# Kernel tuning notes

Hardware: AMD Instinct MI355X
Metric: run time of the kernel (lower is better)

The kernel has to match this reference:

```python
import jax, jax.numpy as jnp
import numpy as np

B, T, C = 16, 512, 1024
D, K, W = 4096, 128, 8


def _scatter_topk(a, k, use_values):
    """Top-k along last axis; return dense array with top-k values (or 1.0) scattered, zeros elsewhere."""
    shp = a.shape
    a2 = a.reshape(-1, shp[-1])
    vals, idx = jax.lax.top_k(a2, k)
    rows = jnp.arange(a2.shape[0])[:, None]
    src = vals if use_values else jnp.ones_like(vals)
    return jnp.zeros_like(a2).at[rows, idx].set(src).reshape(shp)


def _window_topk(x, k, window_size):
    # x: (B, T, D)
    b, t, d = x.shape
    stride = max(1, window_size // 2)
    if stride >= t:
        num_windows, pad, t_pad = 1, 0, t
    else:
        num_windows = (t - window_size) // stride + 1
        required = (num_windows - 1) * stride + window_size
        pad = max(0, required - t)
        t_pad = t + pad
    if pad > 0:
        x = jnp.pad(x, ((0, 0), (0, pad), (0, 0)))
    starts = jnp.arange(num_windows) * stride                      # (NW,)
    tidx = starts[:, None] + jnp.arange(window_size)               # (NW, W)
    x_windows = x[:, tidx, :]                                      # (B, NW, W, D)
    window_sums = x_windows.sum(axis=2)                            # (B, NW, D)
    mask_windows = _scatter_topk(window_sums, k, use_values=False)  # (B, NW, D)
    votes = (x_windows * mask_windows[:, :, None, :]).reshape(b, num_windows * window_size, d)
    feature_votes = jnp.zeros((b, t_pad, d), x.dtype).at[:, tidx.reshape(-1)].add(votes)
    mask_combined = _scatter_topk(feature_votes, k, use_values=False)  # (B, Tp, D)
    x_sparse = x * mask_combined
    return x_sparse[:, :t - 0, :] if pad > 0 else x_sparse


def setup_inputs() -> dict:
    key = jax.random.key(0)
    ks = jax.random.split(key, 4)
    x_ssl = jax.random.normal(ks[0], (B, T, C), jnp.float32)
    W_dec = jax.random.normal(ks[1], (C, D), jnp.float32)
    W_dec = W_dec / jnp.linalg.norm(W_dec, axis=0, keepdims=True)
    W_enc = W_dec.T                                                # tied init, as in module
    W1 = jax.random.normal(ks[2], (256, D), jnp.float32) * (1.0 / np.sqrt(D))
    W2 = jax.random.normal(ks[3], (2, 256), jnp.float32) * (1.0 / np.sqrt(256))
    return dict(
        x_ssl=x_ssl, W_enc=W_enc, b_enc=jnp.zeros((D,), jnp.float32),
        W_dec=W_dec, b_dec=jnp.zeros((C,), jnp.float32),
        ln_g=jnp.ones((D,), jnp.float32), ln_b=jnp.zeros((D,), jnp.float32),
        W1=W1, b1=jnp.zeros((256,), jnp.float32),
        W2=W2, b2=jnp.zeros((2,), jnp.float32),
    )


def reference(x_ssl, W_enc, b_enc, W_dec, b_dec, ln_g, ln_b, W1, b1, W2, b2):
    b, t, c = x_ssl.shape
    x_flat = x_ssl.reshape(b * t, c)
    # SAE encode with window top-k (window_size=8 > 1 path)
    pre = jnp.einsum('nc,dc->nd', x_flat - b_dec, W_enc) + b_enc
    post_relu = jax.nn.relu(pre).reshape(b, t, -1)                 # (B, T, D)
    encoded = _window_topk(post_relu, K, W)                        # (B, T, D)
    encoded_flat = encoded.reshape(b * t, -1)
    # SAE decode + reconstruction loss
    x_recon = jnp.einsum('nd,cd->nc', encoded_flat, W_dec) + b_dec
    sae_loss = jnp.mean((x_recon - x_flat) ** 2)
    # classifier on pooled sparse features (dropout is inference no-op)
    pooled = encoded.mean(axis=1)                                  # (B, D) == AdaptiveAvgPool1d(1)
    mu = pooled.mean(axis=-1, keepdims=True)
    var = pooled.var(axis=-1, keepdims=True)
    ln = (pooled - mu) / jnp.sqrt(var + 1e-5) * ln_g + ln_b
    h = jax.nn.relu(ln @ W1.T + b1)
    logits = h @ W2.T + b2
    log_probs = jax.nn.log_softmax(logits, axis=-1)
    return log_probs, sae_loss
```

## Files before the change

### kernel.cpp

```cpp
#include <hip/hip_runtime.h>

#define BB   16
#define TT   512
#define CC   1024
#define DD   4096
#define NN   (BB*TT)
#define NWIN 127
#define KTOP 128

typedef __attribute__((ext_vector_type(8))) unsigned short ushort8;
typedef _Float16 half8 __attribute__((ext_vector_type(8)));
typedef __attribute__((ext_vector_type(4))) float f32x4;

__device__ __forceinline__ unsigned short f2h(float f) {
    union { _Float16 h; unsigned short u; } c;
    c.h = (_Float16)f;
    return c.u;
}
__device__ __forceinline__ float h2f(unsigned short u) {
    union { unsigned short u; _Float16 h; } c;
    c.u = u;
    return (float)c.h;
}
__device__ __forceinline__ unsigned tokey(float f) {
    unsigned u = __float_as_uint(f);
    return (u & 0x80000000u) ? ~u : (u | 0x80000000u);
}
__device__ __forceinline__ void async_lds16(const void* g, void* l) {
    __builtin_amdgcn_global_load_lds((const __attribute__((address_space(1))) void*)g,
                                     (__attribute__((address_space(3))) void*)l, 16, 0, 0);
}

#define PH_SYNC() do { __builtin_amdgcn_sched_barrier(0); __builtin_amdgcn_s_barrier(); \
                       asm volatile("s_waitcnt lgkmcnt(0)" ::: "memory"); \
                       __builtin_amdgcn_sched_barrier(0); __builtin_amdgcn_s_setprio(1); } while (0)
#define PH_END()  do { __builtin_amdgcn_s_setprio(0); __builtin_amdgcn_sched_barrier(0); \
                       __builtin_amdgcn_s_barrier(); } while (0)

__device__ __forceinline__ unsigned wave_prefix_incl(unsigned v) {
    int lane = threadIdx.x & 63;
#pragma unroll
    for (int off = 1; off < 64; off <<= 1) {
        unsigned n = __shfl_up(v, off, 64);
        if (lane >= off) v += n;
    }
    return v;
}
__device__ __forceinline__ unsigned wave_suffix_incl(unsigned v) {
    int lane = threadIdx.x & 63;
#pragma unroll
    for (int off = 1; off < 64; off <<= 1) {
        unsigned n = __shfl_down(v, off, 64);
        if (lane + off < 64) v += n;
    }
    return v;
}

__device__ __forceinline__ unsigned select_top128(const unsigned* keys,
                                                  unsigned* hist, unsigned* shx) {
    const int tid = threadIdx.x, wid = tid >> 6, lane = tid & 63;
    const unsigned ZKEY = 0x80000000u;
    unsigned cpos = 0, cz = 0;
#pragma unroll
    for (int i = 0; i < 16; ++i) {
        cpos += (keys[i] > ZKEY);
        cz   += (keys[i] == ZKEY);
    }
    unsigned ppos = wave_prefix_incl(cpos);
    unsigned pz   = wave_prefix_incl(cz);
    if (lane == 63) { shx[wid] = ppos; shx[4 + wid] = pz; }
    __syncthreads();
    unsigned nz = shx[0] + shx[1] + shx[2] + shx[3];
    unsigned selbits = 0u;
    if (nz <= KTOP) {
        unsigned need = KTOP - nz;
        unsigned zr = pz - cz;
        if (wid > 0) zr += shx[4];
        if (wid > 1) zr += shx[5];
        if (wid > 2) zr += shx[6];
#pragma unroll
        for (int i = 0; i < 16; ++i) {
            bool sel = (keys[i] > ZKEY) || (keys[i] == ZKEY && zr < need);
            if (keys[i] == ZKEY) ++zr;
            selbits |= (sel ? 1u : 0u) << i;
        }
        return selbits;
    }
    unsigned k2[16];
#pragma unroll
    for (int i = 0; i < 16; ++i) k2[i] = (keys[i] > ZKEY) ? keys[i] : 0u;
    unsigned prefix = 0u, pmask = 0u, Kr = KTOP;
    for (int shift = 24; shift >= 0; shift -= 8) {
        hist[tid] = 0u; hist[256 + tid] = 0u; hist[512 + tid] = 0u; hist[768 + tid] = 0u;
        __syncthreads();
        unsigned* h = hist + (wid << 8);
#pragma unroll
        for (int i = 0; i < 16; ++i)
            if (k2[i] && (k2[i] & pmask) == prefix) atomicAdd(&h[(k2[i] >> shift) & 255u], 1u);
        __syncthreads();
        unsigned v = hist[tid] + hist[256 + tid] + hist[512 + tid] + hist[768 + tid];
        unsigned s = wave_suffix_incl(v);
        if (lane == 0) shx[wid] = s;
        __syncthreads();
        unsigned stot = s;
        if (wid == 0) stot += shx[1] + shx[2] + shx[3];
        else if (wid == 1) stot += shx[2] + shx[3];
        else if (wid == 2) stot += shx[3];
        unsigned above = stot - v;
        if (stot >= Kr && above < Kr) { shx[8] = (unsigned)tid; shx[9] = Kr - above; }
        __syncthreads();
        prefix |= shx[8] << shift;
        pmask |= 0xFFu << shift;
        Kr = shx[9];
    }
    unsigned T = prefix, need = Kr;
    unsigned ce = 0;
#pragma unroll
    for (int i = 0; i < 16; ++i) ce += (k2[i] == T);
    unsigned pe = wave_prefix_incl(ce);
    __syncthreads();
    if (lane == 63) shx[4 + wid] = pe;
    __syncthreads();
    unsigned er = pe - ce;
    if (wid > 0) er += shx[4];
    if (wid > 1) er += shx[5];
    if (wid > 2) er += shx[6];
#pragma unroll
    for (int i = 0; i < 16; ++i) {
        bool sel = (k2[i] > T) || (k2[i] == T && er < need);
        if (k2[i] == T) ++er;
        selbits |= (sel ? 1u : 0u) << i;
    }
    return selbits;
}

__global__ __launch_bounds__(256) void k_convert_all(const float* __restrict__ x,
                                                     const float* __restrict__ Wenc,
                                                     const float* __restrict__ Wdec,
                                                     const float* __restrict__ bdec,
                                                     unsigned short* __restrict__ xh,
                                                     unsigned short* __restrict__ wh,
                                                     unsigned short* __restrict__ wdh,
                                                     float* __restrict__ pooled_zero) {
    const int bid = blockIdx.x;
    if (bid < 8192) {
        size_t i = (size_t)bid * 256 + threadIdx.x;
        float4 v = ((const float4*)x)[i];
        size_t c = (i * 4) & (CC - 1);
        v.x -= bdec[c]; v.y -= bdec[c + 1]; v.z -= bdec[c + 2]; v.w -= bdec[c + 3];
        uint2 o;
        o.x = (unsigned)f2h(v.x) | ((unsigned)f2h(v.y) << 16);
        o.y = (unsigned)f2h(v.z) | ((unsigned)f2h(v.w) << 16);
        ((uint2*)xh)[i] = o;
    } else if (bid < 12288) {
        size_t i = (size_t)(bid - 8192) * 256 + threadIdx.x;
        float4 v = ((const float4*)Wenc)[i];
        uint2 o;
        o.x = (unsigned)f2h(v.x) | ((unsigned)f2h(v.y) << 16);
        o.y = (unsigned)f2h(v.z) | ((unsigned)f2h(v.w) << 16);
        ((uint2*)wh)[i] = o;
    } else if (bid < 16384) {
        size_t i = (size_t)(bid - 12288) * 256 + threadIdx.x;
        float4 v = ((const float4*)Wdec)[i];
        uint2 o;
        o.x = (unsigned)f2h(v.x) | ((unsigned)f2h(v.y) << 16);
        o.y = (unsigned)f2h(v.z) | ((unsigned)f2h(v.w) << 16);
        ((uint2*)wdh)[i] = o;
    } else {
        const int n4 = (BB * DD + 64) / 4;
        for (int i = threadIdx.x; i < n4; i += 256)
            ((float4*)pooled_zero)[i] = make_float4(0.f, 0.f, 0.f, 0.f);
    }
}

__global__ __launch_bounds__(512, 2) void k_gemm_enc_256(const unsigned short* __restrict__ Ah,
                                                         const unsigned short* __restrict__ Bh,
                                                         const float* __restrict__ bias,
                                                         unsigned short* __restrict__ Cout,
                                                         float* __restrict__ gsum) {
    __shared__ __align__(16) unsigned short lds[2][4][128 * 64];
    const int tid = threadIdx.x, w = tid >> 6, lane = tid & 63;
    const int bm = blockIdx.y * 256, bn = blockIdx.x * 256;
    const int wr = w >> 2, wc = w & 3;
    const int rA = lane & 15, q = lane >> 4;
    const int sc0 = (q ^ (rA & 7)) << 3, sc1 = ((4 + q) ^ (rA & 7)) << 3;
    const int s_rt = w * 16 + (lane >> 3);
    const int s_ct = ((lane & 7) ^ (lane >> 3)) * 8;
    const unsigned short* Abase = Ah + ((size_t)(bm + s_rt)) * 1024 + s_ct;
    const unsigned short* Bbase = Bh + ((size_t)(bn + s_rt)) * 1024 + s_ct;

    auto STAGE = [&](const unsigned short* gb, int rowoff, int kt, unsigned short* reg) {
        const unsigned short* g = gb + (size_t)rowoff * 1024 + (kt << 6);
        async_lds16(g, reg + w * 1024);
        async_lds16(g + 8 * 1024, reg + w * 1024 + 512);
    };

    half8 a[4][2], b[4][2];
    f32x4 acc[8][4] = {};

    auto RDA4 = [&](const unsigned short* reg) {
#pragma unroll
        for (int mf = 0; mf < 4; ++mf) {
            const unsigned short* p = reg + (wr * 64 + mf * 16 + rA) * 64;
            a[mf][0] = *(const half8*)(p + sc0);
            a[mf][1] = *(const half8*)(p + sc1);
        }
    };
    auto RDB2 = [&](const unsigned short* reg, int nb) {
#pragma unroll
        for (int nf = 0; nf < 2; ++nf) {
            const unsigned short* p = reg + (wc * 32 + nf * 16 + rA) * 64;
            b[nb + nf][0] = *(const half8*)(p + sc0);
            b[nb + nf][1] = *(const half8*)(p + sc1);
        }
    };
    auto MF = [&](int mb, int nb) {
#pragma unroll
        for (int kk = 0; kk < 2; ++kk)
#pragma unroll
            for (int mf = 0; mf < 4; ++mf)
#pragma unroll
                for (int nf = 0; nf < 2; ++nf)
                    acc[mb + mf][nb + nf] = __builtin_amdgcn_mfma_f32_16x16x32_f16(
                        a[mf][kk], b[nb + nf][kk], acc[mb + mf][nb + nf], 0, 0, 0);
    };

    STAGE(Abase,   0, 0, lds[0][0]);
    STAGE(Bbase,   0, 0, lds[0][2]);
    STAGE(Abase, 128, 0, lds[0][1]);
    STAGE(Bbase, 128, 0, lds[0][3]);
    STAGE(Abase,   0, 1, lds[1][0]);
    STAGE(Bbase,   0, 1, lds[1][2]);
    STAGE(Abase, 128, 1, lds[1][1]);
    asm volatile("s_waitcnt vmcnt(6)" ::: "memory");
    __builtin_amdgcn_s_barrier();

    for (int i = 0; i < 8; ++i) {
        const int ko  = (2 * i + 1) & 15;
        const int ke  = (2 * i + 2) & 15;
        const int ko2 = (2 * i + 3) & 15;
        RDA4(lds[0][0]); RDB2(lds[0][2], 0);
        STAGE(Bbase, 128, ko, lds[1][3]);
        PH_SYNC(); MF(0, 0); PH_END();
        RDB2(lds[0][3], 2);
        STAGE(Abase, 0, ke, lds[0][0]);
        PH_SYNC(); MF(0, 2); PH_END();
        RDA4(lds[0][1]);
        STAGE(Bbase, 0, ke, lds[0][2]);
        PH_SYNC(); MF(4, 0); PH_END();
        STAGE(Abase, 128, ke, lds[0][1]);
        asm volatile("s_waitcnt vmcnt(6)" ::: "memory");
        PH_SYNC(); MF(4, 2); PH_END();
        RDA4(lds[1][0]); RDB2(lds[1][2], 0);
        STAGE(Bbase, 128, ke, lds[0][3]);
        PH_SYNC(); MF(0, 0); PH_END();
        RDB2(lds[1][3], 2);
        STAGE(Abase, 0, ko2, lds[1][0]);
        PH_SYNC(); MF(0, 2); PH_END();
        RDA4(lds[1][1]);
        STAGE(Bbase, 0, ko2, lds[1][2]);
        PH_SYNC(); MF(4, 0); PH_END();
        STAGE(Abase, 128, ko2, lds[1][1]);
        asm volatile("s_waitcnt vmcnt(6)" ::: "memory");
        PH_SYNC(); MF(4, 2); PH_END();
    }

    asm volatile("s_waitcnt vmcnt(0)" ::: "memory");
    __syncthreads();
    float* cbuf = (float*)&lds[0][0][0];
    const int cl = rA, qr = q * 4;
    float bv[4];
#pragma unroll
    for (int nf = 0; nf < 4; ++nf)
        bv[nf] = bias[bn + ((nf < 2) ? wc * 32 + nf * 16 : 128 + wc * 32 + (nf - 2) * 16) + cl];
    const int rg = tid >> 4, seg = tid & 15;
#pragma unroll
    for (int p = 0; p < 2; ++p) {
        if (p) __syncthreads();
#pragma unroll
        for (int mf = 0; mf < 4; ++mf) {
            int lrow0 = wr * 64 + mf * 16 + qr;
#pragma unroll
            for (int nf = 0; nf < 4; ++nf) {
                int col = ((nf < 2) ? wc * 32 + nf * 16 : 128 + wc * 32 + (nf - 2) * 16) + cl;
#pragma unroll
                for (int r = 0; r < 4; ++r) {
                    int lrow = lrow0 + r;
                    float v = acc[p * 4 + mf][nf][r] + bv[nf];
                    v = v > 0.f ? v : 0.f;
                    cbuf[lrow * 256 + (col ^ (((lrow >> 2) & 7) << 2))] = v;
                }
            }
        }
        __syncthreads();
        f32x4 gs0 = {}, gs1 = {}, gs2 = {}, gs3 = {};
#pragma unroll
        for (int i2 = 0; i2 < 4; ++i2) {
            const int lrow = rg * 4 + i2;
            const f32x4* crow = (const f32x4*)cbuf + lrow * 64;
            f32x4 v0 = crow[(seg * 4 + 0) ^ (rg & 7)];
            f32x4 v1 = crow[(seg * 4 + 1) ^ (rg & 7)];
            f32x4 v2 = crow[(seg * 4 + 2) ^ (rg & 7)];
            f32x4 v3 = crow[(seg * 4 + 3) ^ (rg & 7)];
            uint4 o0, o1;
            o0.x = (unsigned)f2h(v0[0]) | ((unsigned)f2h(v0[1]) << 16);
            o0.y = (unsigned)f2h(v0[2]) | ((unsigned)f2h(v0[3]) << 16);
            o0.z = (unsigned)f2h(v1[0]) | ((unsigned)f2h(v1[1]) << 16);
            o0.w = (unsigned)f2h(v1[2]) | ((unsigned)f2h(v1[3]) << 16);
            o1.x = (unsigned)f2h(v2[0]) | ((unsigned)f2h(v2[1]) << 16);
            o1.y = (unsigned)f2h(v2[2]) | ((unsigned)f2h(v2[3]) << 16);
            o1.z = (unsigned)f2h(v3[0]) | ((unsigned)f2h(v3[1]) << 16);
            o1.w = (unsigned)f2h(v3[2]) | ((unsigned)f2h(v3[3]) << 16);
            size_t gr = (size_t)(bm + p * 128 + lrow) * 4096 + bn + seg * 16;
            *(uint4*)&Cout[gr] = o0;
            *(uint4*)&Cout[gr + 8] = o1;
            gs0 += v0; gs1 += v1; gs2 += v2; gs3 += v3;
        }
        if (gsum) {
            size_t gr = ((size_t)(bm >> 2) + p * 32 + rg) * 4096 + bn + seg * 16;
            *(f32x4*)&gsum[gr + 0]  = gs0;
            *(f32x4*)&gsum[gr + 4]  = gs1;
            *(f32x4*)&gsum[gr + 8]  = gs2;
            *(f32x4*)&gsum[gr + 12] = gs3;
        }
    }
}

__global__ __launch_bounds__(512, 2) void k_gemm_recon_256(const unsigned short* __restrict__ Ap,
                                                           const unsigned short* __restrict__ Bp,
                                                           const float* __restrict__ bdec,
                                                           const float* __restrict__ X,
                                                           float* __restrict__ sae) {
    __shared__ __align__(16) unsigned short lds[2][3][128 * 64];
    __shared__ float red[512];
    const int tid = threadIdx.x, w = tid >> 6, lane = tid & 63;
    const int bm = blockIdx.y * 256, bn = blockIdx.x * 128;
    const int wr = w >> 1, wc = w & 1;
    const int rA = lane & 15, q = lane >> 4;
    const int sc0 = (q ^ (rA & 7)) << 3, sc1 = ((4 + q) ^ (rA & 7)) << 3;
    const int s_rt = w * 16 + (lane >> 3);
    const int s_ct = ((lane & 7) ^ (lane >> 3)) * 8;
    const unsigned short* Abase = Ap + ((size_t)(bm + s_rt)) * 4096 + s_ct;
    const unsigned short* Bbase = Bp + ((size_t)(bn + s_rt)) * 4096 + s_ct;

    auto STAGE = [&](const unsigned short* gb, int rowoff, int kt, unsigned short* reg) {
        const unsigned short* g = gb + (size_t)rowoff * 4096 + (kt << 6);
        async_lds16(g, reg + w * 1024);
        async_lds16(g + 8 * 4096, reg + w * 1024 + 512);
    };

    half8 a[2][2], b[4][2];
    f32x4 acc[4][4] = {};

    auto RDA2 = [&](const unsigned short* reg) {
#pragma unroll
        for (int mf = 0; mf < 2; ++mf) {
            const unsigned short* p = reg + (wr * 32 + mf * 16 + rA) * 64;
            a[mf][0] = *(const half8*)(p + sc0);
            a[mf][1] = *(const half8*)(p + sc1);
        }
    };
    auto RDB2 = [&](const unsigned short* reg, int nb) {
#pragma unroll
        for (int nf = 0; nf < 2; ++nf) {
            const unsigned short* p = reg + ((nb ? 64 : 0) + wc * 32 + nf * 16 + rA) * 64;
            b[nb + nf][0] = *(const half8*)(p + sc0);
            b[nb + nf][1] = *(const half8*)(p + sc1);
        }
    };
    auto MF = [&](int mb, int nb) {
#pragma unroll
        for (int kk = 0; kk < 2; ++kk)
#pragma unroll
            for (int mf = 0; mf < 2; ++mf)
#pragma unroll
                for (int nf = 0; nf < 2; ++nf)
                    acc[mb + mf][nb + nf] = __builtin_amdgcn_mfma_f32_16x16x32_f16(
                        a[mf][kk], b[nb + nf][kk], acc[mb + mf][nb + nf], 0, 0, 0);
    };

    STAGE(Abase,   0, 0, lds[0][0]);
    STAGE(Bbase,   0, 0, lds[0][2]);
    STAGE(Abase, 128, 0, lds[0][1]);
    STAGE(Abase,   0, 1, lds[1][0]);
    STAGE(Bbase,   0, 1, lds[1][2]);
    asm volatile("s_waitcnt vmcnt(4)" ::: "memory");
    __builtin_amdgcn_s_barrier();

    for (int i = 0; i < 32; ++i) {
        const int ko  = (2 * i + 1) & 63;
        const int ke  = (2 * i + 2) & 63;
        const int ko2 = (2 * i + 3) & 63;
        RDA2(lds[0][0]); RDB2(lds[0][2], 0);
        STAGE(Abase, 128, ko, lds[1][1]);
        PH_SYNC(); MF(0, 0); PH_END();
        RDB2(lds[0][2], 2);
        STAGE(Abase, 0, ke, lds[0][0]);
        PH_SYNC(); MF(0, 2); PH_END();
        RDA2(lds[0][1]);
        STAGE(Bbase, 0, ke, lds[0][2]);
        PH_SYNC(); MF(2, 0); PH_END();
        asm volatile("s_waitcnt vmcnt(4)" ::: "memory");
        PH_SYNC(); MF(2, 2); PH_END();
        RDA2(lds[1][0]); RDB2(lds[1][2], 0);
        STAGE(Abase, 128, ke, lds[0][1]);
        PH_SYNC(); MF(0, 0); PH_END();
        RDB2(lds[1][2], 2);
        STAGE(Abase, 0, ko2, lds[1][0]);
        PH_SYNC(); MF(0, 2); PH_END();
        RDA2(lds[1][1]);
        STAGE(Bbase, 0, ko2, lds[1][2]);
        PH_SYNC(); MF(2, 0); PH_END();
        asm volatile("s_waitcnt vmcnt(4)" ::: "memory");
        PH_SYNC(); MF(2, 2); PH_END();
    }

    asm volatile("s_waitcnt vmcnt(0)" ::: "memory");
    const int cl = rA, qr = q * 4;
    float lsum = 0.f;
#pragma unroll
    for (int mf = 0; mf < 4; ++mf) {
        int row0 = bm + ((mf < 2) ? wr * 32 + mf * 16 : 128 + wr * 32 + (mf - 2) * 16) + qr;
#pragma unroll
        for (int nf = 0; nf < 4; ++nf) {
            int col = bn + ((nf < 2) ? wc * 32 + nf * 16 : 64 + wc * 32 + (nf - 2) * 16) + cl;
            float bvv = bdec[col];
#pragma unroll
            for (int r = 0; r < 4; ++r) {
                float v = acc[mf][nf][r] + bvv - X[(size_t)(row0 + r) * 1024 + col];
                lsum += v * v;
            }
        }
    }
    red[tid] = lsum;
    __syncthreads();
    for (int s = 256; s > 0; s >>= 1) { if (tid < s) red[tid] += red[tid + s]; __syncthreads(); }
    if (tid == 0) atomicAdd(sae, red[0]);
}

__global__ __launch_bounds__(256) void k_winsum_g(const float* __restrict__ gsum,
                                                  unsigned* __restrict__ wmask) {
    __shared__ unsigned hist[1024];
    __shared__ unsigned shx[16];
    __shared__ unsigned short halves[256];
    const int tid = threadIdx.x, w = blockIdx.x, b = blockIdx.y;
    const float* g0 = gsum + ((size_t)(b * 128 + w)) * DD + tid * 16;
    const float* g1 = g0 + DD;
    unsigned keys[16];
#pragma unroll
    for (int q = 0; q < 4; ++q) {
        float4 u = *(const float4*)(g0 + q * 4);
        float4 v = *(const float4*)(g1 + q * 4);
        keys[q * 4 + 0] = tokey(u.x + v.x);
        keys[q * 4 + 1] = tokey(u.y + v.y);
        keys[q * 4 + 2] = tokey(u.z + v.z);
        keys[q * 4 + 3] = tokey(u.w + v.w);
    }
    unsigned selbits = select_top128(keys, hist, shx);
    halves[tid] = (unsigned short)selbits;
    __syncthreads();
    if (tid < 128)
        wmask[(size_t)(b * NWIN + w) * 128 + tid] =
            (unsigned)halves[2 * tid] | ((unsigned)halves[2 * tid + 1] << 16);
}

__global__ __launch_bounds__(256) void k_winsum_p(const unsigned short* __restrict__ post,
                                                  unsigned* __restrict__ wmask) {
    __shared__ unsigned hist[1024];
    __shared__ unsigned shx[16];
    __shared__ unsigned short halves[256];
    const int tid = threadIdx.x, w = blockIdx.x, b = blockIdx.y;
    const unsigned short* base = post + (size_t)(b * TT + w * 4) * DD + tid * 16;
    float s[16] = {};
#pragma unroll
    for (int j = 0; j < 8; ++j) {
        const unsigned short* rp = base + (size_t)j * DD;
        ushort8 u0 = *(const ushort8*)rp;
        ushort8 u1 = *(const ushort8*)(rp + 8);
#pragma unroll
        for (int i = 0; i < 8; ++i) { s[i] += h2f(u0[i]); s[8 + i] += h2f(u1[i]); }
    }
    unsigned keys[16];
#pragma unroll
    for (int i = 0; i < 16; ++i) keys[i] = tokey(s[i]);
    unsigned selbits = select_top128(keys, hist, shx);
    halves[tid] = (unsigned short)selbits;
    __syncthreads();
    if (tid < 128)
        wmask[(size_t)(b * NWIN + w) * 128 + tid] =
            (unsigned)halves[2 * tid] | ((unsigned)halves[2 * tid + 1] << 16);
}

__global__ __launch_bounds__(256) void k_votes(unsigned short* __restrict__ post,
                                               const unsigned* __restrict__ wmask,
                                               float* __restrict__ pooled) {
    __shared__ unsigned long long cand[256];
    __shared__ unsigned char selbyte[DD];
    __shared__ unsigned shx[16];
    __shared__ unsigned hcnt[256];
    const int tid = threadIdx.x, wid = tid >> 6, lane = tid & 63;
    const int g = blockIdx.x, b = blockIdx.y;
    int w1 = g, w0 = g - 1;
    unsigned mw0 = 0u, mw1 = 0u;
    if (w0 >= 0)        mw0 = wmask[(size_t)(b * NWIN + w0) * 128 + (tid >> 1)];
    if (w1 <= NWIN - 1) mw1 = wmask[(size_t)(b * NWIN + w1) * 128 + (tid >> 1)];
    const int bbase = (tid & 1) * 16;
    const unsigned ZKEY = 0x80000000u;
    float psum[16];
#pragma unroll
    for (int i = 0; i < 16; ++i) psum[i] = 0.f;

    for (int r = 0; r < 4; ++r) {
        unsigned short* rp = post + (size_t)(b * TT + g * 4 + r) * DD;
        ushort8 raw0 = *(const ushort8*)(rp + tid * 16);
        ushort8 raw1 = *(const ushort8*)(rp + tid * 16 + 8);
        float vals[16];
#pragma unroll
        for (int i = 0; i < 8; ++i) { vals[i] = h2f(raw0[i]); vals[8 + i] = h2f(raw1[i]); }
        unsigned keys[16];
#pragma unroll
        for (int i = 0; i < 16; ++i) {
            float cov = (float)(((mw0 >> (bbase + i)) & 1u) + ((mw1 >> (bbase + i)) & 1u));
            keys[i] = tokey(vals[i] * cov);
        }
        unsigned cpos = 0, cz = 0;
#pragma unroll
        for (int i = 0; i < 16; ++i) {
            cpos += (keys[i] > ZKEY);
            cz   += (keys[i] == ZKEY);
        }
        unsigned ppos = wave_prefix_incl(cpos);
        unsigned pz   = wave_prefix_incl(cz);
        __syncthreads();
        if (lane == 63) { shx[wid] = ppos; shx[4 + wid] = pz; }
        __syncthreads();
        unsigned nz = shx[0] + shx[1] + shx[2] + shx[3];
        unsigned selbits = 0u;
        if (nz <= KTOP) {
            unsigned need = KTOP - nz;
            unsigned zr = pz - cz;
            if (wid > 0) zr += shx[4];
            if (wid > 1) zr += shx[5];
            if (wid > 2) zr += shx[6];
#pragma unroll
            for (int i = 0; i < 16; ++i) {
                bool sel = (keys[i] > ZKEY) || (keys[i] == ZKEY && zr < need);
                if (keys[i] == ZKEY) ++zr;
                selbits |= (sel ? 1u : 0u) << i;
            }
        } else {
            *(uint4*)(selbyte + tid * 16) = make_uint4(0u, 0u, 0u, 0u);
            unsigned off = ppos - cpos;
            if (wid > 0) off += shx[0];
            if (wid > 1) off += shx[1];
            if (wid > 2) off += shx[2];
#pragma unroll
            for (int i = 0; i < 16; ++i) {
                if (keys[i] > ZKEY && off < 256u) {
                    int d = tid * 16 + i;
                    cand[off++] = ((unsigned long long)keys[i] << 12) | (unsigned)(4095 - d);
                }
            }
            __syncthreads();
            const unsigned m = nz < 256u ? nz : 256u;
            unsigned long long ek = (tid < (int)m) ? cand[tid] : 0ULL;
            unsigned Kr = KTOP;
            bool alive = (tid < (int)m);
            bool sel = false;
#pragma unroll
            for (int pass = 0; pass < 3; ++pass) {
                const int shift = 36 - pass * 8;
                hcnt[tid] = 0u;
                __syncthreads();
                unsigned dg = (unsigned)(ek >> shift) & 255u;
                if (alive) atomicAdd(&hcnt[dg], 1u);
                __syncthreads();
                unsigned v = hcnt[tid];
                unsigned s = wave_suffix_incl(v);
                if (lane == 0) shx[8 + wid] = s;
                __syncthreads();
                unsigned stot = s;
                if (wid == 0) stot += shx[9] + shx[10] + shx[11];
                else if (wid == 1) stot += shx[10] + shx[11];
                else if (wid == 2) stot += shx[11];
                unsigned above = stot - v;
                if (stot >= Kr && above < Kr) { shx[12] = (unsigned)tid; shx[13] = Kr - above; }
                __syncthreads();
                unsigned Td = shx[12];
                Kr = shx[13];
                if (alive) {
                    if (dg > Td) { sel = true; alive = false; }
                    else if (dg < Td) alive = false;
                }
            }
            unsigned av = alive ? 1u : 0u;
            unsigned pa = wave_prefix_incl(av);
            if (lane == 63) shx[8 + wid] = pa;
            __syncthreads();
            unsigned er = pa - av;
            if (wid > 0) er += shx[8];
            if (wid > 1) er += shx[9];
            if (wid > 2) er += shx[10];
            if (alive && er < Kr) sel = true;
            if (sel) selbyte[4095 - (unsigned)(ek & 0xFFFu)] = 1;
            __syncthreads();
#pragma unroll
            for (int i = 0; i < 16; ++i)
                selbits |= (selbyte[tid * 16 + i] ? 1u : 0u) << i;
        }
        ushort8 o0, o1;
#pragma unroll
        for (int i = 0; i < 8; ++i) {
            bool s0 = (selbits >> i) & 1u;
            bool s1 = (selbits >> (8 + i)) & 1u;
            o0[i] = s0 ? raw0[i] : (unsigned short)0;
            o1[i] = s1 ? raw1[i] : (unsigned short)0;
            if (s0) psum[i]     += vals[i];
            if (s1) psum[8 + i] += vals[8 + i];
        }
        *(ushort8*)(rp + tid * 16)     = o0;
        *(ushort8*)(rp + tid * 16 + 8) = o1;
    }
#pragma unroll
    for (int i = 0; i < 16; ++i)
        if (psum[i] != 0.f) atomicAdd(&pooled[(size_t)b * DD + tid * 16 + i], psum[i]);
}

__device__ __forceinline__ float block_sum(float v, float* red) {
    const int tid = threadIdx.x;
    red[tid] = v;
    __syncthreads();
    for (int s = 128; s > 0; s >>= 1) { if (tid < s) red[tid] += red[tid + s]; __syncthreads(); }
    float r = red[0];
    __syncthreads();
    return r;
}

__global__ __launch_bounds__(256) void k_head_ln(const float* __restrict__ pooled,
                                                 const float* __restrict__ lng,
                                                 const float* __restrict__ lnb,
                                                 float* __restrict__ lnout) {
    __shared__ float red[256];
    const int b = blockIdx.x, tid = threadIdx.x;
    float pv[16];
    float s = 0.f;
#pragma unroll
    for (int q = 0; q < 4; ++q) {
        float4 u = *(const float4*)(pooled + (size_t)b * DD + tid * 16 + q * 4);
        pv[q * 4 + 0] = u.x * (1.f / TT); pv[q * 4 + 1] = u.y * (1.f / TT);
        pv[q * 4 + 2] = u.z * (1.f / TT); pv[q * 4 + 3] = u.w * (1.f / TT);
        s += pv[q * 4 + 0] + pv[q * 4 + 1] + pv[q * 4 + 2] + pv[q * 4 + 3];
    }
    float mean = block_sum(s, red) * (1.f / (float)DD);
    float vs = 0.f;
#pragma unroll
    for (int i = 0; i < 16; ++i) { float c = pv[i] - mean; vs += c * c; }
    float var = block_sum(vs, red) * (1.f / (float)DD);
    float inv = rsqrtf(var + 1e-5f);
#pragma unroll
    for (int q = 0; q < 4; ++q) {
        float4 g = *(const float4*)(lng + tid * 16 + q * 4);
        float4 bb = *(const float4*)(lnb + tid * 16 + q * 4);
        float4 o;
        o.x = (pv[q * 4 + 0] - mean) * inv * g.x + bb.x;
        o.y = (pv[q * 4 + 1] - mean) * inv * g.y + bb.y;
        o.z = (pv[q * 4 + 2] - mean) * inv * g.z + bb.z;
        o.w = (pv[q * 4 + 3] - mean) * inv * g.w + bb.w;
        *(float4*)(lnout + (size_t)b * DD + tid * 16 + q * 4) = o;
    }
}

__global__ __launch_bounds__(256) void k_head_mlp(const float* __restrict__ lnout,
                                                  const float* __restrict__ W1,
                                                  const float* __restrict__ b1,
                                                  float* __restrict__ h) {
    const int gw = (blockIdx.x * 256 + threadIdx.x) >> 6;
    const int lane = threadIdx.x & 63;
    const int b = gw >> 8, row = gw & 255;
    const float* lp = lnout + (size_t)b * DD;
    const float* wr = W1 + (size_t)row * DD;
    float a = 0.f;
#pragma unroll
    for (int k = 0; k < DD / 64; ++k)
        a += lp[lane + 64 * k] * wr[lane + 64 * k];
#pragma unroll
    for (int off = 32; off > 0; off >>= 1) a += __shfl_down(a, off, 64);
    if (lane == 0) h[b * 256 + row] = fmaxf(a + b1[row], 0.f);
}

__global__ __launch_bounds__(256) void k_head_out(const float* __restrict__ h,
                                                  const float* __restrict__ W2,
                                                  const float* __restrict__ b2,
                                                  const float* __restrict__ sae,
                                                  float* __restrict__ out) {
    __shared__ float red[256];
    const int b = blockIdx.x, tid = threadIdx.x;
    float hv = h[b * 256 + tid];
    float l0 = block_sum(hv * W2[tid], red) + b2[0];
    float l1 = block_sum(hv * W2[256 + tid], red) + b2[1];
    if (tid == 0) {
        float m = fmaxf(l0, l1);
        float lse = m + logf(expf(l0 - m) + expf(l1 - m));
        out[2 * b] = l0 - lse;
        out[2 * b + 1] = l1 - lse;
        if (b == 0) out[32] = sae[0] * (1.f / (float)((size_t)NN * CC));
    }
}

extern "C" void kernel_launch(void* const* d_in, const int* in_sizes, int n_in,
                              void* d_out, int out_size, void* d_ws, size_t ws_size,
                              hipStream_t stream) {
    const float* x    = (const float*)d_in[0];
    const float* Wenc = (const float*)d_in[1];
    const float* benc = (const float*)d_in[2];
    const float* Wdec = (const float*)d_in[3];
    const float* bdec = (const float*)d_in[4];
    const float* lng  = (const float*)d_in[5];
    const float* lnb  = (const float*)d_in[6];
    const float* W1   = (const float*)d_in[7];
    const float* b1   = (const float*)d_in[8];
    const float* W2   = (const float*)d_in[9];
    const float* b2   = (const float*)d_in[10];
    float* out = (float*)d_out;

    char* ws = (char*)d_ws;
    unsigned short* post  = (unsigned short*)(ws + 0);
    unsigned short* xh16  = (unsigned short*)(ws + 67108864);
    unsigned short* scr   = (unsigned short*)(ws + 83886080);
    unsigned short* wh16  = (unsigned short*)(ws + 100663296);
    unsigned short* wd16  = (unsigned short*)(ws + 109051904);
    unsigned*       wmask = (unsigned*)(ws + 117440512);
    float*          pooled= (float*)(ws + 118480896);
    float*          sae   = (float*)(ws + 118743040);
    float*          gsum  = (float*)(ws + 118743296);
    const bool use_gsum = ws_size >= (size_t)118743296 + 33554432;
    float* gptr = use_gsum ? gsum : nullptr;
    float* lnout = (float*)xh16;
    float* hbuf  = (float*)scr;

    k_convert_all<<<dim3(16385), 256, 0, stream>>>(x, Wenc, Wdec, bdec, xh16, wh16, wd16, pooled);

    k_gemm_enc_256<<<dim3(DD / 256, NN / 256), 512, 0, stream>>>(xh16, wh16, benc, post, gptr);
    if (use_gsum)
        k_winsum_g<<<dim3(NWIN, BB), 256, 0, stream>>>(gsum, wmask);
    else
        k_winsum_p<<<dim3(NWIN, BB), 256, 0, stream>>>(post, wmask);
    k_votes<<<dim3(TT / 4, BB), 256, 0, stream>>>(post, wmask, pooled);
    k_gemm_recon_256<<<dim3(CC / 128, NN / 256), 512, 0, stream>>>(post, wd16, bdec, x, sae);
    k_head_ln<<<dim3(BB), 256, 0, stream>>>(pooled, lng, lnb, lnout);
    k_head_mlp<<<dim3(1024), 256, 0, stream>>>(lnout, W1, b1, hbuf);
    k_head_out<<<dim3(BB), 256, 0, stream>>>(hbuf, W2, b2, sae, out);
}
```

Baseline: 423.6 us.

## Load A fragments directly to registers and stage only B through LDS

Both the encoder and decoder GEMMs stop staging A tiles through LDS. Each wave now loads its A fragments straight from global memory into registers, double-buffered as even and odd sets, while only B goes through async LDS copies with a simpler two-buffer vmcnt(0)+barrier gate. The wave layout changes so each wave owns 64 rows and a wider column span, and the encoder epilogue writes in four passes. This is meant to cut LDS traffic and barrier count, at the cost of uncoalesced global A loads, higher register pressure and fully exposed load latency at each gate.

```diff
diff --git a/kernel.cpp b/kernel.cpp
--- a/kernel.cpp
+++ b/kernel.cpp
@@ -31,11 +31,10 @@
                                      (__attribute__((address_space(3))) void*)l, 16, 0, 0);
 }
 
-#define PH_SYNC() do { __builtin_amdgcn_sched_barrier(0); __builtin_amdgcn_s_barrier(); \
-                       asm volatile("s_waitcnt lgkmcnt(0)" ::: "memory"); \
-                       __builtin_amdgcn_sched_barrier(0); __builtin_amdgcn_s_setprio(1); } while (0)
-#define PH_END()  do { __builtin_amdgcn_s_setprio(0); __builtin_amdgcn_sched_barrier(0); \
-                       __builtin_amdgcn_s_barrier(); } while (0)
+#define GATE() do { __builtin_amdgcn_sched_barrier(0); \
+                    asm volatile("s_waitcnt vmcnt(0)" ::: "memory"); \
+                    __builtin_amdgcn_s_barrier(); \
+                    __builtin_amdgcn_sched_barrier(0); } while (0)
 
 __device__ __forceinline__ unsigned wave_prefix_incl(unsigned v) {
     int lane = threadIdx.x & 63;
@@ -173,155 +172,146 @@
     }
 }
 
+__device__ __forceinline__ void stage256(const unsigned short* gbase, size_t ldk,
+                                         unsigned short* lds, int w, int lane) {
+    const int sub = lane >> 3;
+    const int cj  = (lane & 7) ^ sub;
+#pragma unroll
+    for (int i = 0; i < 4; ++i) {
+        int n = w * 4 + i;
+        int r = n * 8 + sub;
+        async_lds16(gbase + (size_t)r * ldk + cj * 8, lds + n * 512);
+    }
+}
+__device__ __forceinline__ void stage128(const unsigned short* gbase, size_t ldk,
+                                         unsigned short* lds, int w, int lane) {
+    const int sub = lane >> 3;
+    const int cj  = (lane & 7) ^ sub;
+#pragma unroll
+    for (int i = 0; i < 2; ++i) {
+        int n = w * 2 + i;
+        int r = n * 8 + sub;
+        async_lds16(gbase + (size_t)r * ldk + cj * 8, lds + n * 512);
+    }
+}
+
 __global__ __launch_bounds__(512, 2) void k_gemm_enc_256(const unsigned short* __restrict__ Ah,
                                                          const unsigned short* __restrict__ Bh,
                                                          const float* __restrict__ bias,
                                                          unsigned short* __restrict__ Cout,
                                                          float* __restrict__ gsum) {
-    __shared__ __align__(16) unsigned short lds[2][4][128 * 64];
+    __shared__ __align__(16) unsigned short Bt[2][2][128 * 64];
     const int tid = threadIdx.x, w = tid >> 6, lane = tid & 63;
     const int bm = blockIdx.y * 256, bn = blockIdx.x * 256;
-    const int wr = w >> 2, wc = w & 3;
+    const int wr = w >> 1, wc = w & 1;
     const int rA = lane & 15, q = lane >> 4;
     const int sc0 = (q ^ (rA & 7)) << 3, sc1 = ((4 + q) ^ (rA & 7)) << 3;
-    const int s_rt = w * 16 + (lane >> 3);
-    const int s_ct = ((lane & 7) ^ (lane >> 3)) * 8;
-    const unsigned short* Abase = Ah + ((size_t)(bm + s_rt)) * 1024 + s_ct;
-    const unsigned short* Bbase = Bh + ((size_t)(bn + s_rt)) * 1024 + s_ct;
-
-    auto STAGE = [&](const unsigned short* gb, int rowoff, int kt, unsigned short* reg) {
-        const unsigned short* g = gb + (size_t)rowoff * 1024 + (kt << 6);
-        async_lds16(g, reg + w * 1024);
-        async_lds16(g + 8 * 1024, reg + w * 1024 + 512);
+    const unsigned short* Braw = Bh + (size_t)bn * 1024;
+    const unsigned short* Agp  = Ah + ((size_t)(bm + wr * 64 + rA)) * 1024 + q * 8;
+
+    half8 aE[4][2], aO[4][2];
+    f32x4 acc[4][8] = {};
+
+    auto LDA = [&](half8 (&dst)[4][2], int kt) {
+        const unsigned short* g = Agp + (kt << 6);
+#pragma unroll
+        for (int mf = 0; mf < 4; ++mf)
+#pragma unroll
+            for (int kk = 0; kk < 2; ++kk)
+                dst[mf][kk] = *(const half8*)(g + (size_t)mf * 16 * 1024 + kk * 32);
     };
-
-    half8 a[4][2], b[4][2];
-    f32x4 acc[8][4] = {};
-
-    auto RDA4 = [&](const unsigned short* reg) {
-#pragma unroll
-        for (int mf = 0; mf < 4; ++mf) {
-            const unsigned short* p = reg + (wr * 64 + mf * 16 + rA) * 64;
-            a[mf][0] = *(const half8*)(p + sc0);
-            a[mf][1] = *(const half8*)(p + sc1);
-        }
+    auto STAGEB = [&](int kt, unsigned short* buf) {
+        stage256(Braw + (kt << 6), 1024, buf, w, lane);
     };
-    auto RDB2 = [&](const unsigned short* reg, int nb) {
-#pragma unroll
-        for (int nf = 0; nf < 2; ++nf) {
-            const unsigned short* p = reg + (wc * 32 + nf * 16 + rA) * 64;
-            b[nb + nf][0] = *(const half8*)(p + sc0);
-            b[nb + nf][1] = *(const half8*)(p + sc1);
-        }
+    auto CL = [&](half8 (&aC)[4][2], const unsigned short* rb, int c) {
+        half8 b[2][2];
+#pragma unroll
+        for (int j = 0; j < 2; ++j) {
+            const unsigned short* p = rb + ((2 * c + j) * 16 + rA) * 64;
+            b[j][0] = *(const half8*)(p + sc0);
+            b[j][1] = *(const half8*)(p + sc1);
+        }
+        __builtin_amdgcn_s_setprio(1);
+#pragma unroll
+        for (int kk = 0; kk < 2; ++kk)
+#pragma unroll
+            for (int mf = 0; mf < 4; ++mf)
+#pragma unroll
+                for (int j = 0; j < 2; ++j)
+                    acc[mf][2 * c + j] = __builtin_amdgcn_mfma_f32_16x16x32_f16(
+                        aC[mf][kk], b[j][kk], acc[mf][2 * c + j], 0, 0, 0);
+        __builtin_amdgcn_s_setprio(0);
     };
-    auto MF = [&](int mb, int nb) {
-#pragma unroll
-        for (int kk = 0; kk < 2; ++kk)
-#pragma unroll
-            for (int mf = 0; mf < 4; ++mf)
-#pragma unroll
-                for (int nf = 0; nf < 2; ++nf)
-                    acc[mb + mf][nb + nf] = __builtin_amdgcn_mfma_f32_16x16x32_f16(
-                        a[mf][kk], b[nb + nf][kk], acc[mb + mf][nb + nf], 0, 0, 0);
-    };
-
-    STAGE(Abase,   0, 0, lds[0][0]);
-    STAGE(Bbase,   0, 0, lds[0][2]);
-    STAGE(Abase, 128, 0, lds[0][1]);
-    STAGE(Bbase, 128, 0, lds[0][3]);
-    STAGE(Abase,   0, 1, lds[1][0]);
-    STAGE(Bbase,   0, 1, lds[1][2]);
-    STAGE(Abase, 128, 1, lds[1][1]);
-    asm volatile("s_waitcnt vmcnt(6)" ::: "memory");
-    __builtin_amdgcn_s_barrier();
-
+
+    LDA(aE, 0);
+    STAGEB(0, &Bt[0][0][0]);
+
+#pragma unroll 1
     for (int i = 0; i < 8; ++i) {
-        const int ko  = (2 * i + 1) & 15;
-        const int ke  = (2 * i + 2) & 15;
-        const int ko2 = (2 * i + 3) & 15;
-        RDA4(lds[0][0]); RDB2(lds[0][2], 0);
-        STAGE(Bbase, 128, ko, lds[1][3]);
-        PH_SYNC(); MF(0, 0); PH_END();
-        RDB2(lds[0][3], 2);
-        STAGE(Abase, 0, ke, lds[0][0]);
-        PH_SYNC(); MF(0, 2); PH_END();
-        RDA4(lds[0][1]);
-        STAGE(Bbase, 0, ke, lds[0][2]);
-        PH_SYNC(); MF(4, 0); PH_END();
-        STAGE(Abase, 128, ke, lds[0][1]);
-        asm volatile("s_waitcnt vmcnt(6)" ::: "memory");
-        PH_SYNC(); MF(4, 2); PH_END();
-        RDA4(lds[1][0]); RDB2(lds[1][2], 0);
-        STAGE(Bbase, 128, ke, lds[0][3]);
-        PH_SYNC(); MF(0, 0); PH_END();
-        RDB2(lds[1][3], 2);
-        STAGE(Abase, 0, ko2, lds[1][0]);
-        PH_SYNC(); MF(0, 2); PH_END();
-        RDA4(lds[1][1]);
-        STAGE(Bbase, 0, ko2, lds[1][2]);
-        PH_SYNC(); MF(4, 0); PH_END();
-        STAGE(Abase, 128, ko2, lds[1][1]);
-        asm volatile("s_waitcnt vmcnt(6)" ::: "memory");
-        PH_SYNC(); MF(4, 2); PH_END();
-    }
-
-    asm volatile("s_waitcnt vmcnt(0)" ::: "memory");
-    __syncthreads();
-    float* cbuf = (float*)&lds[0][0][0];
+        const int t0 = 2 * i, t1 = 2 * i + 1;
+        GATE();
+        { LDA(aO, t0 + 1); STAGEB(t0 + 1, &Bt[1][0][0]); }
+        __builtin_amdgcn_sched_barrier(0);
+        {
+            const unsigned short* rb = &Bt[0][wc][0];
+            CL(aE, rb, 0); CL(aE, rb, 1); CL(aE, rb, 2); CL(aE, rb, 3);
+        }
+        GATE();
+        if (t1 + 1 < 16) { LDA(aE, t1 + 1); STAGEB(t1 + 1, &Bt[0][0][0]); }
+        __builtin_amdgcn_sched_barrier(0);
+        {
+            const unsigned short* rb = &Bt[1][wc][0];
+            CL(aO, rb, 0); CL(aO, rb, 1); CL(aO, rb, 2); CL(aO, rb, 3);
+        }
+    }
+
+    __syncthreads();
+    float* cbuf = (float*)&Bt[0][0][0];
     const int cl = rA, qr = q * 4;
-    float bv[4];
-#pragma unroll
-    for (int nf = 0; nf < 4; ++nf)
-        bv[nf] = bias[bn + ((nf < 2) ? wc * 32 + nf * 16 : 128 + wc * 32 + (nf - 2) * 16) + cl];
-    const int rg = tid >> 4, seg = tid & 15;
-#pragma unroll
-    for (int p = 0; p < 2; ++p) {
+    float bv[8];
+#pragma unroll
+    for (int nf = 0; nf < 8; ++nf) bv[nf] = bias[bn + wc * 128 + nf * 16 + cl];
+    const int rg = tid >> 5, seg = tid & 31;
+#pragma unroll 1
+    for (int p = 0; p < 4; ++p) {
         if (p) __syncthreads();
-#pragma unroll
-        for (int mf = 0; mf < 4; ++mf) {
-            int lrow0 = wr * 64 + mf * 16 + qr;
-#pragma unroll
-            for (int nf = 0; nf < 4; ++nf) {
-                int col = ((nf < 2) ? wc * 32 + nf * 16 : 128 + wc * 32 + (nf - 2) * 16) + cl;
-#pragma unroll
-                for (int r = 0; r < 4; ++r) {
-                    int lrow = lrow0 + r;
-                    float v = acc[p * 4 + mf][nf][r] + bv[nf];
-                    v = v > 0.f ? v : 0.f;
-                    cbuf[lrow * 256 + (col ^ (((lrow >> 2) & 7) << 2))] = v;
+        if (wr == p) {
+#pragma unroll
+            for (int mf = 0; mf < 4; ++mf) {
+#pragma unroll
+                for (int nf = 0; nf < 8; ++nf) {
+                    int col = wc * 128 + nf * 16 + cl;
+#pragma unroll
+                    for (int r = 0; r < 4; ++r) {
+                        int lrow = mf * 16 + qr + r;
+                        float v = acc[mf][nf][r] + bv[nf];
+                        v = v > 0.f ? v : 0.f;
+                        cbuf[lrow * 256 + (col ^ (((lrow >> 2) & 7) << 2))] = v;
+                    }
                 }
             }
         }
         __syncthreads();
-        f32x4 gs0 = {}, gs1 = {}, gs2 = {}, gs3 = {};
+        f32x4 gs0 = {}, gs1 = {};
 #pragma unroll
         for (int i2 = 0; i2 < 4; ++i2) {
             const int lrow = rg * 4 + i2;
             const f32x4* crow = (const f32x4*)cbuf + lrow * 64;
-            f32x4 v0 = crow[(seg * 4 + 0) ^ (rg & 7)];
-            f32x4 v1 = crow[(seg * 4 + 1) ^ (rg & 7)];
-            f32x4 v2 = crow[(seg * 4 + 2) ^ (rg & 7)];
-            f32x4 v3 = crow[(seg * 4 + 3) ^ (rg & 7)];
-            uint4 o0, o1;
-            o0.x = (unsigned)f2h(v0[0]) | ((unsigned)f2h(v0[1]) << 16);
-            o0.y = (unsigned)f2h(v0[2]) | ((unsigned)f2h(v0[3]) << 16);
-            o0.z = (unsigned)f2h(v1[0]) | ((unsigned)f2h(v1[1]) << 16);
-            o0.w = (unsigned)f2h(v1[2]) | ((unsigned)f2h(v1[3]) << 16);
-            o1.x = (unsigned)f2h(v2[0]) | ((unsigned)f2h(v2[1]) << 16);
-            o1.y = (unsigned)f2h(v2[2]) | ((unsigned)f2h(v2[3]) << 16);
-            o1.z = (unsigned)f2h(v3[0]) | ((unsigned)f2h(v3[1]) << 16);
-            o1.w = (unsigned)f2h(v3[2]) | ((unsigned)f2h(v3[3]) << 16);
-            size_t gr = (size_t)(bm + p * 128 + lrow) * 4096 + bn + seg * 16;
-            *(uint4*)&Cout[gr] = o0;
-            *(uint4*)&Cout[gr + 8] = o1;
-            gs0 += v0; gs1 += v1; gs2 += v2; gs3 += v3;
+            const int s = (lrow >> 2) & 7;
+            f32x4 v0 = crow[(seg * 2 + 0) ^ s];
+            f32x4 v1 = crow[(seg * 2 + 1) ^ s];
+            uint4 o;
+            o.x = (unsigned)f2h(v0[0]) | ((unsigned)f2h(v0[1]) << 16);
+            o.y = (unsigned)f2h(v0[2]) | ((unsigned)f2h(v0[3]) << 16);
+            o.z = (unsigned)f2h(v1[0]) | ((unsigned)f2h(v1[1]) << 16);
+            o.w = (unsigned)f2h(v1[2]) | ((unsigned)f2h(v1[3]) << 16);
+            *(uint4*)&Cout[(size_t)(bm + p * 64 + lrow) * 4096 + bn + seg * 8] = o;
+            gs0 += v0; gs1 += v1;
         }
         if (gsum) {
-            size_t gr = ((size_t)(bm >> 2) + p * 32 + rg) * 4096 + bn + seg * 16;
-            *(f32x4*)&gsum[gr + 0]  = gs0;
-            *(f32x4*)&gsum[gr + 4]  = gs1;
-            *(f32x4*)&gsum[gr + 8]  = gs2;
-            *(f32x4*)&gsum[gr + 12] = gs3;
+            size_t gr = ((size_t)(bm >> 2) + p * 16 + rg) * 4096 + bn + seg * 8;
+            *(f32x4*)&gsum[gr + 0] = gs0;
+            *(f32x4*)&gsum[gr + 4] = gs1;
         }
     }
 }
@@ -331,99 +321,71 @@
                                                            const float* __restrict__ bdec,
                                                            const float* __restrict__ X,
                                                            float* __restrict__ sae) {
-    __shared__ __align__(16) unsigned short lds[2][3][128 * 64];
+    __shared__ __align__(16) unsigned short Bt[2][128 * 64];
     __shared__ float red[512];
     const int tid = threadIdx.x, w = tid >> 6, lane = tid & 63;
     const int bm = blockIdx.y * 256, bn = blockIdx.x * 128;
     const int wr = w >> 1, wc = w & 1;
     const int rA = lane & 15, q = lane >> 4;
     const int sc0 = (q ^ (rA & 7)) << 3, sc1 = ((4 + q) ^ (rA & 7)) << 3;
-    const int s_rt = w * 16 + (lane >> 3);
-    const int s_ct = ((lane & 7) ^ (lane >> 3)) * 8;
-    const unsigned short* Abase = Ap + ((size_t)(bm + s_rt)) * 4096 + s_ct;
-    const unsigned short* Bbase = Bp + ((size_t)(bn + s_rt)) * 4096 + s_ct;
-
-    auto STAGE = [&](const unsigned short* gb, int rowoff, int kt, unsigned short* reg) {
-        const unsigned short* g = gb + (size_t)rowoff * 4096 + (kt << 6);
-        async_lds16(g, reg + w * 1024);
-        async_lds16(g + 8 * 4096, reg + w * 1024 + 512);
+    const unsigned short* Braw = Bp + (size_t)bn * 4096;
+    const unsigned short* Agp  = Ap + ((size_t)(bm + wr * 64 + rA)) * 4096 + q * 8;
+
+    half8 aE[4][2], aO[4][2];
+    f32x4 acc[4][4] = {};
+
+    auto LDA = [&](half8 (&dst)[4][2], int kt) {
+        const unsigned short* g = Agp + (kt << 6);
+#pragma unroll
+        for (int mf = 0; mf < 4; ++mf)
+#pragma unroll
+            for (int kk = 0; kk < 2; ++kk)
+                dst[mf][kk] = *(const half8*)(g + (size_t)mf * 16 * 4096 + kk * 32);
     };
-
-    half8 a[2][2], b[4][2];
-    f32x4 acc[4][4] = {};
-
-    auto RDA2 = [&](const unsigned short* reg) {
-#pragma unroll
-        for (int mf = 0; mf < 2; ++mf) {
-            const unsigned short* p = reg + (wr * 32 + mf * 16 + rA) * 64;
-            a[mf][0] = *(const half8*)(p + sc0);
-            a[mf][1] = *(const half8*)(p + sc1);
-        }
+    auto CL = [&](half8 (&aC)[4][2], const unsigned short* rb, int c) {
+        half8 b[2][2];
+#pragma unroll
+        for (int j = 0; j < 2; ++j) {
+            const unsigned short* p = rb + (wc * 64 + (2 * c + j) * 16 + rA) * 64;
+            b[j][0] = *(const half8*)(p + sc0);
+            b[j][1] = *(const half8*)(p + sc1);
+        }
+        __builtin_amdgcn_s_setprio(1);
+#pragma unroll
+        for (int kk = 0; kk < 2; ++kk)
+#pragma unroll
+            for (int mf = 0; mf < 4; ++mf)
+#pragma unroll
+                for (int j = 0; j < 2; ++j)
+                    acc[mf][2 * c + j] = __builtin_amdgcn_mfma_f32_16x16x32_f16(
+                        aC[mf][kk], b[j][kk], acc[mf][2 * c + j], 0, 0, 0);
+        __builtin_amdgcn_s_setprio(0);
     };
-    auto RDB2 = [&](const unsigned short* reg, int nb) {
-#pragma unroll
-        for (int nf = 0; nf < 2; ++nf) {
-            const unsigned short* p = reg + ((nb ? 64 : 0) + wc * 32 + nf * 16 + rA) * 64;
-            b[nb + nf][0] = *(const half8*)(p + sc0);
-            b[nb + nf][1] = *(const half8*)(p + sc1);
-        }
-    };
-    auto MF = [&](int mb, int nb) {
-#pragma unroll
-        for (int kk = 0; kk < 2; ++kk)
-#pragma unroll
-            for (int mf = 0; mf < 2; ++mf)
-#pragma unroll
-                for (int nf = 0; nf < 2; ++nf)
-                    acc[mb + mf][nb + nf] = __builtin_amdgcn_mfma_f32_16x16x32_f16(
-                        a[mf][kk], b[nb + nf][kk], acc[mb + mf][nb + nf], 0, 0, 0);
-    };
-
-    STAGE(Abase,   0, 0, lds[0][0]);
-    STAGE(Bbase,   0, 0, lds[0][2]);
-    STAGE(Abase, 128, 0, lds[0][1]);
-    STAGE(Abase,   0, 1, lds[1][0]);
-    STAGE(Bbase,   0, 1, lds[1][2]);
-    asm volatile("s_waitcnt vmcnt(4)" ::: "memory");
-    __builtin_amdgcn_s_barrier();
-
+
+    LDA(aE, 0);
+    stage128(Braw, 4096, &Bt[0][0], w, lane);
+
+#pragma unroll 1
     for (int i = 0; i < 32; ++i) {
-        const int ko  = (2 * i + 1) & 63;
-        const int ke  = (2 * i + 2) & 63;
-        const int ko2 = (2 * i + 3) & 63;
-        RDA2(lds[0][0]); RDB2(lds[0][2], 0);
-        STAGE(Abase, 128, ko, lds[1][1]);
-        PH_SYNC(); MF(0, 0); PH_END();
-        RDB2(lds[0][2], 2);
-        STAGE(Abase, 0, ke, lds[0][0]);
-        PH_SYNC(); MF(0, 2); PH_END();
-        RDA2(lds[0][1]);
-        STAGE(Bbase, 0, ke, lds[0][2]);
-        PH_SYNC(); MF(2, 0); PH_END();
-        asm volatile("s_waitcnt vmcnt(4)" ::: "memory");
-        PH_SYNC(); MF(2, 2); PH_END();
-        RDA2(lds[1][0]); RDB2(lds[1][2], 0);
-        STAGE(Abase, 128, ke, lds[0][1]);
-        PH_SYNC(); MF(0, 0); PH_END();
-        RDB2(lds[1][2], 2);
-        STAGE(Abase, 0, ko2, lds[1][0]);
-        PH_SYNC(); MF(0, 2); PH_END();
-        RDA2(lds[1][1]);
-        STAGE(Bbase, 0, ko2, lds[1][2]);
-        PH_SYNC(); MF(2, 0); PH_END();
-        asm volatile("s_waitcnt vmcnt(4)" ::: "memory");
-        PH_SYNC(); MF(2, 2); PH_END();
-    }
-
-    asm volatile("s_waitcnt vmcnt(0)" ::: "memory");
+        const int t0 = 2 * i, t1 = 2 * i + 1;
+        GATE();
+        { LDA(aO, t0 + 1); stage128(Braw + ((t0 + 1) << 6), 4096, &Bt[1][0], w, lane); }
+        __builtin_amdgcn_sched_barrier(0);
+        { const unsigned short* rb = &Bt[0][0]; CL(aE, rb, 0); CL(aE, rb, 1); }
+        GATE();
+        if (t1 + 1 < 64) { LDA(aE, t1 + 1); stage128(Braw + ((t1 + 1) << 6), 4096, &Bt[0][0], w, lane); }
+        __builtin_amdgcn_sched_barrier(0);
+        { const unsigned short* rb = &Bt[1][0]; CL(aO, rb, 0); CL(aO, rb, 1); }
+    }
+
     const int cl = rA, qr = q * 4;
     float lsum = 0.f;
 #pragma unroll
     for (int mf = 0; mf < 4; ++mf) {
-        int row0 = bm + ((mf < 2) ? wr * 32 + mf * 16 : 128 + wr * 32 + (mf - 2) * 16) + qr;
+        int row0 = bm + wr * 64 + mf * 16 + qr;
 #pragma unroll
         for (int nf = 0; nf < 4; ++nf) {
-            int col = bn + ((nf < 2) ? wc * 32 + nf * 16 : 64 + wc * 32 + (nf - 2) * 16) + cl;
+            int col = bn + wc * 64 + nf * 16 + cl;
             float bvv = bdec[col];
 #pragma unroll
             for (int r = 0; r < 4; ++r) {
```

Result: slower. 531.9 us (+25.6%).
